# Performance work log

Hardware: AMD Instinct MI355X
Metric: run time of the kernel (lower is better)

The kernel has to match this reference:

```python
import jax, jax.numpy as jnp
import numpy as np
from jax import lax

D = 256      # key/query dim
D_F = 256    # diff feature channels
C_TOK = 1    # leading context tokens in query_vit
EPS = 1e-6


def conv2d(x, w, b, pad):
    out = lax.conv_general_dilated(x, w, (1, 1), [(pad, pad), (pad, pad)],
                                   dimension_numbers=('NCHW', 'OIHW', 'NCHW'))
    return out + b[None, :, None, None]


def gn1(x, g, b):
    # GroupNorm with 1 group: normalize over (C,H,W) per sample
    mu = jnp.mean(x, axis=(1, 2, 3), keepdims=True)
    var = jnp.var(x, axis=(1, 2, 3), keepdims=True)
    xn = (x - mu) * lax.rsqrt(var + EPS)
    return xn * g[None, :, None, None] + b[None, :, None, None]


def resize_bilinear_ac(x, Ho, Wo):
    # F.interpolate(mode='bilinear', align_corners=True)
    B, C, H, W = x.shape
    ys = jnp.linspace(0.0, H - 1.0, Ho)
    xs = jnp.linspace(0.0, W - 1.0, Wo)
    y0 = jnp.floor(ys).astype(jnp.int32)
    y1 = jnp.minimum(y0 + 1, H - 1)
    wy = (ys - y0)[None, None, :, None]
    x0 = jnp.floor(xs).astype(jnp.int32)
    x1 = jnp.minimum(x0 + 1, W - 1)
    wx = (xs - x0)[None, None, None, :]
    r = x[:, :, y0, :] * (1.0 - wy) + x[:, :, y1, :] * wy
    return r[:, :, :, x0] * (1.0 - wx) + r[:, :, :, x1] * wx


def setup_inputs() -> dict:
    key = jax.random.key(0)
    ks = jax.random.split(key, 12)
    B, Hd, Wd, Ht, Wt = 8, 64, 64, 32, 32

    def kaiming(k, shape, fan_in):
        return jax.random.normal(k, shape, jnp.float32) * np.sqrt(2.0 / fan_in)

    return {
        'query_vit': jax.random.normal(ks[0], (B, C_TOK + Ht * Wt, D), jnp.float32),
        'feat_diff_cat': jax.random.normal(ks[1], (B, 5 * D_F, Hd, Wd), jnp.float32),
        'rb_w1': kaiming(ks[2], (D_F, 5 * D_F, 3, 3), 5 * D_F * 9), 'rb_b1': jnp.zeros((D_F,), jnp.float32),
        'rb_w2': kaiming(ks[3], (D_F, D_F, 3, 3), D_F * 9), 'rb_b2': jnp.zeros((D_F,), jnp.float32),
        'rb_ws': kaiming(ks[4], (D_F, 5 * D_F, 1, 1), 5 * D_F), 'rb_bs': jnp.zeros((D_F,), jnp.float32),
        'ln_g': jnp.ones((D_F,), jnp.float32), 'ln_b': jnp.zeros((D_F,), jnp.float32),
        'key_w': kaiming(ks[5], (D, D_F, 1, 1), D_F), 'key_b': jnp.zeros((D,), jnp.float32),
        'val_w': kaiming(ks[6], (D_F, D_F, 1, 1), D_F), 'val_b': jnp.zeros((D_F,), jnp.float32),
        'dh0_w': kaiming(ks[7], (D_F, D_F, 3, 3), D_F * 9), 'dh0_b': jnp.zeros((D_F,), jnp.float32),
        'dh1_w': kaiming(ks[8], (D_F, D_F, 3, 3), D_F * 9), 'dh1_b': jnp.zeros((D_F,), jnp.float32),
    }


def reference(query_vit, feat_diff_cat, rb_w1, rb_b1, rb_w2, rb_b2, rb_ws, rb_bs,
              ln_g, ln_b, key_w, key_b, val_w, val_b, dh0_w, dh0_b, dh1_w, dh1_b):
    B, _, h_diff, w_diff = feat_diff_cat.shape
    N = query_vit.shape[1] - C_TOK
    h_trm = w_trm = int(N ** 0.5)

    # ResBlock_ysh(D_f*5 -> D_f): conv3x3 + relu + conv3x3, 1x1-projected residual
    h = jax.nn.relu(conv2d(feat_diff_cat, rb_w1, rb_b1, 1))
    h = conv2d(h, rb_w2, rb_b2, 1)
    feat_diff = jax.nn.relu(h + conv2d(feat_diff_cat, rb_ws, rb_bs, 0))

    fln = gn1(feat_diff, ln_g, ln_b)
    key_diff = conv2d(fln, key_w, key_b, 0).reshape(B, D, -1)          # (B, D, HW)
    value_diff = conv2d(fln, val_w, val_b, 0).reshape(B, D_F, -1)      # (B, Df, HW)
    value_diff = jnp.transpose(value_diff, (0, 2, 1))                  # (B, HW, Df)

    # cross attention: (B, C+N, D) @ (B, D, HW) -> softmax -> @ (B, HW, Df)
    scores = jnp.einsum('bnd,bdm->bnm', query_vit, key_diff) * (D ** -0.5)
    attn = jax.nn.softmax(scores, axis=-1)
    out_cross = jnp.einsum('bnm,bmf->bnf', attn, value_diff)           # (B, C+N, Df)

    out_cross_c = out_cross[:, :C_TOK, :]
    out_p = jnp.transpose(out_cross[:, C_TOK:, :], (0, 2, 1)).reshape(B, D_F, h_trm, w_trm)
    out_p = jax.nn.relu(conv2d(out_p, dh0_w, dh0_b, 1))
    out_p = resize_bilinear_ac(out_p, h_diff, w_diff)
    out_p = out_p + feat_diff                                          # DropPath(0) = identity
    out_p = jax.nn.relu(conv2d(gn1(out_p, ln_g, ln_b), dh1_w, dh1_b, 1)) + out_p
    return out_cross_c, out_p
```

## Files before the change

kernel.cpp:

```cpp
#include <hip/hip_runtime.h>
#include <cstdint>
#include <cstddef>

typedef __attribute__((ext_vector_type(4))) float     f32x4;
typedef __attribute__((ext_vector_type(8))) __bf16    bf16x8;
typedef __attribute__((ext_vector_type(8))) short     short8;
typedef __attribute__((ext_vector_type(4))) unsigned short u16x4;
typedef unsigned short u16;

__device__ __forceinline__ float b2f(u16 u) {
  unsigned x = ((unsigned)u) << 16;
  float f;
  __builtin_memcpy(&f, &x, 4);
  return f;
}
__device__ __forceinline__ u16 f2b(float f) {
  unsigned u;
  __builtin_memcpy(&u, &f, 4);
  return (u16)((u + 0x7FFFu + ((u >> 16) & 1u)) >> 16);
}

struct GP {
  const u16*  A;
  const u16*  B;
  const float* bias;
  const void* aux;
  void*       C;
  float*      out0;
  long long   aBS, bBS, cBS, auxBS;
  int Ktot, Mrows, ldc;
  int cin, logW, wpad, poff;
  float scale;
};

#define GLDS16(g, l)                                                        \
  __builtin_amdgcn_global_load_lds(                                         \
      (const void __attribute__((address_space(1)))*)(g),                   \
      (void __attribute__((address_space(3)))*)(l), 16, 0, 0)

template <int AMODE, int CW, bool RELU>
__global__ __launch_bounds__(512, 2) void k_gemm8(GP gp) {
  const int tid = threadIdx.x;
  const int l = tid & 63, w = tid >> 6;
  const int b = blockIdx.z;
  const int m0 = blockIdx.x * 128;
  const int wm = w >> 2, wn = w & 3;

  __shared__ __align__(16) u16 sm[3][24576];

  f32x4 acc[4][4];
#pragma unroll
  for (int i = 0; i < 4; ++i)
#pragma unroll
    for (int j = 0; j < 4; ++j) acc[i][j] = (f32x4){0.f, 0.f, 0.f, 0.f};

  const u16* Ab = gp.A + (size_t)b * gp.aBS;
  const u16* Bb = gp.B + (size_t)b * gp.bBS;
  const int scoff = (((tid & 7) ^ ((tid >> 3) & 7)) << 3);

  const u16* aP[2];
  const u16* bP[4];
#pragma unroll
  for (int i = 0; i < 2; ++i) {
    const int p = m0 + i * 64 + (tid >> 3);
    if (AMODE == 0) {
      const int pc = p < gp.Mrows ? p : gp.Mrows - 1;
      aP[i] = Ab + (size_t)pc * gp.Ktot + scoff;
    } else {
      const int y = p >> gp.logW, x = p & ((1 << gp.logW) - 1);
      aP[i] = Ab + (size_t)((y + gp.poff) * gp.wpad + (x + gp.poff)) * gp.cin +
              scoff;
    }
  }
#pragma unroll
  for (int i = 0; i < 4; ++i)
    bP[i] = Bb + (size_t)(i * 64 + (tid >> 3)) * gp.Ktot + scoff;

  const int NT = gp.Ktot >> 6;
  int kcS = 0, tapS = 0, dxS = 0, ktS = 0;

  auto adv = [&](int& kA, int& kB) {
    kB = ktS << 6;
    if (AMODE == 0) {
      kA = ktS << 6;
    } else {
      kA = tapS * gp.cin + kcS;
      kcS += 64;
      if (kcS == gp.cin) {
        kcS = 0; ++dxS; ++tapS;
        if (dxS == 3) { dxS = 0; tapS += gp.wpad - 3; }
      }
    }
    ++ktS;
  };

#pragma unroll
  for (int pt = 0; pt < 2; ++pt) {
    int kA, kB;
    adv(kA, kB);
    u16* sA = &sm[pt][0] + (w << 9);
    u16* sB = &sm[pt][8192] + (w << 9);
    GLDS16(aP[0] + kA, sA);
    GLDS16(aP[1] + kA, sA + 4096);
    GLDS16(bP[0] + kB, sB);
    GLDS16(bP[1] + kB, sB + 4096);
    GLDS16(bP[2] + kB, sB + 8192);
    GLDS16(bP[3] + kB, sB + 12288);
  }
  asm volatile("s_waitcnt vmcnt(6)" ::: "memory");
  __builtin_amdgcn_s_barrier();

  const int lr = l & 15, lc = l >> 4;
  int bufC = 0, bufS = 2;

  for (int t = 0; t < NT; ++t) {
    const u16* sAc = &sm[bufC][0];
    const u16* sBc = &sm[bufC][8192];
    const bool sOK = (t + 2 < NT);
    int kAs = 0, kBs = 0;
    if (sOK) adv(kAs, kBs);
    u16* sAs = &sm[bufS][0] + (w << 9);
    u16* sBs = &sm[bufS][8192] + (w << 9);

    bf16x8 bv[4][2];
    {
      bf16x8 av[2][2];
#pragma unroll
      for (int mi = 0; mi < 2; ++mi) {
        const int row = wm * 64 + mi * 16 + lr;
#pragma unroll
        for (int ks = 0; ks < 2; ++ks) {
          const int cc = ks * 4 + lc;
          av[mi][ks] =
              *(const bf16x8*)(sAc + row * 64 + ((cc ^ (row & 7)) << 3));
        }
      }
#pragma unroll
      for (int ni = 0; ni < 4; ++ni) {
        const int row = wn * 64 + ni * 16 + lr;
#pragma unroll
        for (int ks = 0; ks < 2; ++ks) {
          const int cc = ks * 4 + lc;
          bv[ni][ks] =
              *(const bf16x8*)(sBc + row * 64 + ((cc ^ (row & 7)) << 3));
        }
      }
      if (sOK) {
        GLDS16(aP[0] + kAs, sAs);
        GLDS16(aP[1] + kAs, sAs + 4096);
        GLDS16(bP[0] + kBs, sBs);
      }
      __builtin_amdgcn_s_barrier();
      asm volatile("s_waitcnt lgkmcnt(0)" ::: "memory");
      __builtin_amdgcn_sched_barrier(0);
      __builtin_amdgcn_s_setprio(1);
#pragma unroll
      for (int ks = 0; ks < 2; ++ks)
#pragma unroll
        for (int mi = 0; mi < 2; ++mi)
#pragma unroll
          for (int ni = 0; ni < 4; ++ni)
            acc[mi][ni] = __builtin_amdgcn_mfma_f32_16x16x32_bf16(
                av[mi][ks], bv[ni][ks], acc[mi][ni], 0, 0, 0);
      __builtin_amdgcn_sched_barrier(0);
      __builtin_amdgcn_s_setprio(0);
    }
    __builtin_amdgcn_s_barrier();
    {
      bf16x8 av[2][2];
#pragma unroll
      for (int mi = 0; mi < 2; ++mi) {
        const int row = wm * 64 + (mi + 2) * 16 + lr;
#pragma unroll
        for (int ks = 0; ks < 2; ++ks) {
          const int cc = ks * 4 + lc;
          av[mi][ks] =
              *(const bf16x8*)(sAc + row * 64 + ((cc ^ (row & 7)) << 3));
        }
      }
      if (sOK) {
        GLDS16(bP[1] + kBs, sBs + 4096);
        GLDS16(bP[2] + kBs, sBs + 8192);
        GLDS16(bP[3] + kBs, sBs + 12288);
      }
      __builtin_amdgcn_s_barrier();
      asm volatile("s_waitcnt lgkmcnt(0)" ::: "memory");
      __builtin_amdgcn_sched_barrier(0);
      __builtin_amdgcn_s_setprio(1);
#pragma unroll
      for (int ks = 0; ks < 2; ++ks)
#pragma unroll
        for (int mi = 0; mi < 2; ++mi)
#pragma unroll
          for (int ni = 0; ni < 4; ++ni)
            acc[mi + 2][ni] = __builtin_amdgcn_mfma_f32_16x16x32_bf16(
                av[mi][ks], bv[ni][ks], acc[mi + 2][ni], 0, 0, 0);
      __builtin_amdgcn_sched_barrier(0);
      __builtin_amdgcn_s_setprio(0);
    }
    if (t + 1 < NT) {
      if (t + 2 < NT)
        asm volatile("s_waitcnt vmcnt(6)" ::: "memory");
      else
        asm volatile("s_waitcnt vmcnt(0)" ::: "memory");
      __builtin_amdgcn_s_barrier();
    }
    bufC = bufC == 2 ? 0 : bufC + 1;
    bufS = bufS == 2 ? 0 : bufS + 1;
  }

#pragma unroll
  for (int mi = 0; mi < 4; ++mi) {
#pragma unroll
    for (int ni = 0; ni < 4; ++ni) {
      const int ncol = wn * 64 + ni * 16 + lr;
      const int mbase = m0 + wm * 64 + mi * 16 + lc * 4;
      const float bv_ = gp.bias ? gp.bias[ncol] : 0.f;
      if constexpr (CW == 0) {
#pragma unroll
        for (int r = 0; r < 4; ++r) {
          float v = acc[mi][ni][r] + bv_;
          if (RELU) v = fmaxf(v, 0.f);
          ((u16*)gp.C)[(size_t)b * gp.cBS + (size_t)(mbase + r) * 256 + ncol] =
              f2b(v);
        }
      } else if constexpr (CW == 1) {
#pragma unroll
        for (int r = 0; r < 4; ++r) {
          float v = acc[mi][ni][r] + bv_;
          if (RELU) v = fmaxf(v, 0.f);
          const int mrow = mbase + r;
          const int y = mrow >> 6, x = mrow & 63;
          ((u16*)gp.C)[(size_t)b * gp.cBS +
                       (size_t)((y + 1) * 66 + x + 1) * 256 + ncol] = f2b(v);
        }
      } else if constexpr (CW == 2) {
#pragma unroll
        for (int r = 0; r < 4; ++r) {
          const int mrow = mbase + r;
          const float s =
              b2f(((const u16*)gp.aux)[(size_t)b * gp.auxBS +
                                       (size_t)mrow * 256 + ncol]);
          float v = acc[mi][ni][r] + bv_ + s;
          v = fmaxf(v, 0.f);
          ((float*)gp.C)[(size_t)b * gp.cBS + (size_t)mrow * 256 + ncol] = v;
        }
      } else if constexpr (CW == 6) {
        float* Cf =
            (float*)gp.C + (size_t)b * gp.cBS + (size_t)ncol * 4096 + mbase;
        const float* mid = (const float*)gp.aux + (size_t)b * gp.auxBS;
        f32x4 o;
#pragma unroll
        for (int r = 0; r < 4; ++r) {
          float v = acc[mi][ni][r] + bv_;
          v = fmaxf(v, 0.f);
          o[r] = v + mid[(size_t)(mbase + r) * 256 + ncol];
        }
        *(f32x4*)Cf = o;
      }
    }
  }
}

template <int AMODE, int CW, bool RELU>
__global__ __launch_bounds__(256, 2) void k_gemm(GP gp) {
  const int tid = threadIdx.x;
  const int l = tid & 63, w = tid >> 6;
  const int b = blockIdx.z;
  const int m0 = blockIdx.x * 128, n0 = blockIdx.y * 128;
  const int wm = w >> 1, wn = w & 1;

  __shared__ __align__(16) u16 smA[128 * 64];
  __shared__ __align__(16) u16 smB[128 * 64];

  f32x4 acc[4][4];
#pragma unroll
  for (int i = 0; i < 4; ++i)
#pragma unroll
    for (int j = 0; j < 4; ++j) acc[i][j] = (f32x4){0.f, 0.f, 0.f, 0.f};

  const u16* Ab = gp.A + (size_t)b * gp.aBS;
  const u16* Bb = gp.B + (size_t)b * gp.bBS;

  const int scoff = (((l & 7) ^ (l >> 3)) << 3);

  const u16* aRow[4];
  const u16* bRow[4];
  u16* ldsA[4];
  u16* ldsB[4];
#pragma unroll
  for (int i = 0; i < 4; ++i) {
    const int r = w * 32 + i * 8 + (l >> 3);
    bRow[i] = Bb + (size_t)(n0 + r) * gp.Ktot + scoff;
    const int p = m0 + r;
    if (AMODE == 0) {
      const int pc = p < gp.Mrows ? p : gp.Mrows - 1;
      aRow[i] = Ab + (size_t)pc * gp.Ktot + scoff;
    } else {
      const int y = p >> gp.logW, x = p & ((1 << gp.logW) - 1);
      const int icoord = (y + gp.poff) * gp.wpad + (x + gp.poff);
      aRow[i] = Ab + (size_t)icoord * gp.cin + scoff;
    }
    ldsA[i] = smA + (w * 32 + i * 8) * 64;
    ldsB[i] = smB + (w * 32 + i * 8) * 64;
  }

  const int ktiles = gp.Ktot >> 6;
  int tap_off = 0, dx = 0, kc = 0;

  for (int kt = 0; kt < ktiles; ++kt) {
    int koffA;
    if (AMODE == 0)
      koffA = kt << 6;
    else
      koffA = tap_off * gp.cin + kc;
    const int koffB = kt << 6;
#pragma unroll
    for (int i = 0; i < 4; ++i) GLDS16(aRow[i] + koffA, ldsA[i]);
#pragma unroll
    for (int i = 0; i < 4; ++i) GLDS16(bRow[i] + koffB, ldsB[i]);

    if (AMODE == 1) {
      kc += 64;
      if (kc == gp.cin) {
        kc = 0;
        ++dx;
        ++tap_off;
        if (dx == 3) { dx = 0; tap_off += gp.wpad - 3; }
      }
    }

    __syncthreads();
#pragma unroll
    for (int ks = 0; ks < 2; ++ks) {
      bf16x8 av[4], bv[4];
      const int cc = (ks << 2) + (l >> 4);
#pragma unroll
      for (int mi = 0; mi < 4; ++mi) {
        const int row = wm * 64 + mi * 16 + (l & 15);
        av[mi] = *(const bf16x8*)((const char*)smA + (row << 7) +
                                  ((cc ^ (row & 7)) << 4));
      }
#pragma unroll
      for (int ni = 0; ni < 4; ++ni) {
        const int row = wn * 64 + ni * 16 + (l & 15);
        bv[ni] = *(const bf16x8*)((const char*)smB + (row << 7) +
                                  ((cc ^ (row & 7)) << 4));
      }
#pragma unroll
      for (int mi = 0; mi < 4; ++mi)
#pragma unroll
        for (int ni = 0; ni < 4; ++ni)
          acc[mi][ni] = __builtin_amdgcn_mfma_f32_16x16x32_bf16(
              av[mi], bv[ni], acc[mi][ni], 0, 0, 0);
    }
    __syncthreads();
  }

#pragma unroll
  for (int mi = 0; mi < 4; ++mi) {
#pragma unroll
    for (int ni = 0; ni < 4; ++ni) {
      const int ncol = n0 + wn * 64 + ni * 16 + (l & 15);
      const int mbase = m0 + wm * 64 + mi * 16 + ((l >> 4) << 2);
      const float bv_ = gp.bias ? gp.bias[ncol] : 0.f;

      if constexpr (CW == 3) {
        u16* Cu = (u16*)gp.C + (size_t)b * gp.cBS + (size_t)ncol * 4096 + mbase;
        u16x4 pk;
#pragma unroll
        for (int r = 0; r < 4; ++r) pk[r] = f2b(acc[mi][ni][r] + bv_);
        *(u16x4*)Cu = pk;
      } else if constexpr (CW == 7) {
        u16* base = (u16*)gp.C;
        if (ncol < 256) {
#pragma unroll
          for (int r = 0; r < 4; ++r)
            base[(size_t)b * 1048576 + (size_t)(mbase + r) * 256 + ncol] =
                f2b(acc[mi][ni][r] + bv_);
        } else {
          u16x4 pk;
#pragma unroll
          for (int r = 0; r < 4; ++r) pk[r] = f2b(acc[mi][ni][r] + bv_);
          *(u16x4*)(base + 8388608 + (size_t)b * 1048576 +
                    (size_t)(ncol - 256) * 4096 + mbase) = pk;
        }
      } else if constexpr (CW == 6) {
        float* Cf = (float*)gp.C + (size_t)b * gp.cBS + (size_t)ncol * 4096 + mbase;
        const float* mid = (const float*)gp.aux + (size_t)b * gp.auxBS;
        f32x4 o;
#pragma unroll
        for (int r = 0; r < 4; ++r) {
          float v = acc[mi][ni][r] + bv_;
          v = v > 0.f ? v : 0.f;
          o[r] = v + mid[(size_t)(mbase + r) * 256 + ncol];
        }
        *(f32x4*)Cf = o;
      } else {
#pragma unroll
        for (int reg = 0; reg < 4; ++reg) {
          const int mrow = mbase + reg;
          if (mrow >= gp.Mrows) continue;
          float v = acc[mi][ni][reg] * gp.scale + bv_;
          if (RELU) v = v > 0.f ? v : 0.f;
          if constexpr (CW == 0) {
            ((u16*)gp.C)[(size_t)b * gp.cBS + (size_t)mrow * gp.ldc + ncol] =
                f2b(v);
          } else if constexpr (CW == 2) {
            const float s =
                b2f(((const u16*)gp.aux)[(size_t)b * gp.auxBS +
                                         (size_t)mrow * 256 + ncol]);
            float v2 = v + s;
            v2 = v2 > 0.f ? v2 : 0.f;
            ((float*)gp.C)[(size_t)b * gp.cBS + (size_t)mrow * 256 + ncol] = v2;
          } else if constexpr (CW == 4) {
            if (mrow == 0) {
              gp.out0[(size_t)b * 256 + ncol] = v;
            } else {
              const int p = mrow - 1, y = p >> 5, x = p & 31;
              ((u16*)gp.C)[(size_t)b * gp.cBS +
                           (size_t)((y + 1) * 34 + (x + 1)) * 256 + ncol] =
                  f2b(v);
            }
          } else if constexpr (CW == 5) {
            ((float*)gp.C)[(size_t)b * gp.cBS + (size_t)mrow * 256 + ncol] = v;
          }
        }
      }
    }
  }
}


__global__ __launch_bounds__(256) void k_prep_x(const float* __restrict__ x,
                                                u16* __restrict__ o) {
  __shared__ float t[32][65];
  const int b = blockIdx.z, c0 = blockIdx.y << 5, y = blockIdx.x;
  const float* src = x + ((size_t)b * 1280 + c0) * 4096 + (size_t)y * 64;
#pragma unroll
  for (int i = 0; i < 8; ++i) {
    const int idx = threadIdx.x + (i << 8);
    const int c = idx >> 6, xx = idx & 63;
    t[c][xx] = src[(size_t)c * 4096 + xx];
  }
  __syncthreads();
  u16* dst = o + ((size_t)b * 4356 + (size_t)(y + 1) * 66 + 1) * 1280 + c0;
#pragma unroll
  for (int i = 0; i < 8; ++i) {
    const int idx = threadIdx.x + (i << 8);
    const int xx = idx >> 5, c = idx & 31;
    dst[(size_t)xx * 1280 + c] = f2b(t[c][xx]);
  }
}

__global__ __launch_bounds__(256) void k_zero_border(u16* __restrict__ p,
                                                     int P, int C) {
  const int per_img = (4 * P - 4) * C;
  const int total = 8 * per_img;
  for (int idx = blockIdx.x * 256 + threadIdx.x; idx < total;
       idx += gridDim.x * 256) {
    const int b = idx / per_img;
    const int r = idx % per_img;
    const int pix = r / C, c = r % C;
    int y, x;
    const int Pm = P - 1;
    if (pix < P) { y = 0; x = pix; }
    else if (pix < 2 * P) { y = Pm; x = pix - P; }
    else if (pix < 3 * P - 2) { y = pix - 2 * P + 1; x = 0; }
    else { y = pix - (3 * P - 2) + 1; x = Pm; }
    p[((size_t)b * P * P + (size_t)y * P + x) * C + c] = 0;
  }
}

__global__ __launch_bounds__(256) void k_prep_w3(const float* __restrict__ w,
                                                 u16* __restrict__ o, int cin,
                                                 int n) {
  for (int i = blockIdx.x * 256 + threadIdx.x; i < n; i += gridDim.x * 256) {
    const int ci = i % cin;
    const int r = i / cin;
    const int t = r % 9;
    const int co = r / 9;
    o[i] = f2b(w[((size_t)co * cin + ci) * 9 + t]);
  }
}

__global__ __launch_bounds__(256) void k_f2b(const float* __restrict__ x,
                                             u16* __restrict__ o, int n) {
  for (int i = blockIdx.x * 256 + threadIdx.x; i < n; i += gridDim.x * 256)
    o[i] = f2b(x[i]);
}

__global__ __launch_bounds__(256) void k_gn_stats(const float* __restrict__ x,
                                                  float* __restrict__ st) {
  const int b = blockIdx.y;
  const f32x4* xb = (const f32x4*)(x + (size_t)b * 1048576);
  float s = 0.f, s2 = 0.f;
  for (int i = blockIdx.x * 256 + threadIdx.x; i < 262144;
       i += gridDim.x * 256) {
    const f32x4 v = xb[i];
    s += v[0] + v[1] + v[2] + v[3];
    s2 += v[0] * v[0] + v[1] * v[1] + v[2] * v[2] + v[3] * v[3];
  }
#pragma unroll
  for (int o = 32; o; o >>= 1) {
    s += __shfl_down(s, o);
    s2 += __shfl_down(s2, o);
  }
  __shared__ float ls[4], ls2[4];
  const int w = threadIdx.x >> 6;
  if ((threadIdx.x & 63) == 0) { ls[w] = s; ls2[w] = s2; }
  __syncthreads();
  if (threadIdx.x == 0) {
    atomicAdd(&st[b * 2], ls[0] + ls[1] + ls[2] + ls[3]);
    atomicAdd(&st[b * 2 + 1], ls2[0] + ls2[1] + ls2[2] + ls2[3]);
  }
}

template <bool PAD>
__global__ __launch_bounds__(256) void k_gn_norm(const float* __restrict__ x,
                                                 const float* __restrict__ st,
                                                 const float* __restrict__ g,
                                                 const float* __restrict__ bb,
                                                 u16* __restrict__ o) {
  const int b = blockIdx.y;
  const float mu = st[b * 2] * (1.f / 1048576.f);
  const float var = st[b * 2 + 1] * (1.f / 1048576.f) - mu * mu;
  const float rs = rsqrtf(var + 1e-6f);
  const int i4 = blockIdx.x * 256 + threadIdx.x;
  const f32x4 v = ((const f32x4*)(x + (size_t)b * 1048576))[i4];
  const int flat = i4 << 2;
  const int c = flat & 255;
  const int p = flat >> 8;
  const f32x4 gv = *(const f32x4*)(g + c);
  const f32x4 bv = *(const f32x4*)(bb + c);
  u16x4 r;
#pragma unroll
  for (int k = 0; k < 4; ++k) r[k] = f2b((v[k] - mu) * rs * gv[k] + bv[k]);
  size_t oidx;
  if (PAD) {
    const int y = p >> 6, xx = p & 63;
    oidx = ((size_t)b * 4356 + (size_t)(y + 1) * 66 + xx + 1) * 256 + c;
  } else {
    oidx = ((size_t)b * 4096 + p) * 256 + c;
  }
  *(u16x4*)(o + oidx) = r;
}

__global__ __launch_bounds__(256) void k_softmax(u16* __restrict__ s) {
  const size_t row = blockIdx.x;
  u16* p = s + row * 4096;
  const int t = threadIdx.x;
  const short8 r0 = ((const short8*)p)[t];
  const short8 r1 = ((const short8*)p)[t + 256];
  float v[16];
#pragma unroll
  for (int i = 0; i < 8; ++i) {
    v[i] = b2f((u16)r0[i]);
    v[8 + i] = b2f((u16)r1[i]);
  }
  float m = v[0];
#pragma unroll
  for (int i = 1; i < 16; ++i) m = fmaxf(m, v[i]);
#pragma unroll
  for (int o = 32; o; o >>= 1) m = fmaxf(m, __shfl_xor(m, o));
  __shared__ float lm[4], lsum[4];
  const int w = t >> 6;
  if ((t & 63) == 0) lm[w] = m;
  __syncthreads();
  m = fmaxf(fmaxf(lm[0], lm[1]), fmaxf(lm[2], lm[3]));
  float sum = 0.f;
#pragma unroll
  for (int i = 0; i < 16; ++i) {
    v[i] = __expf(v[i] - m);
    sum += v[i];
  }
#pragma unroll
  for (int o = 32; o; o >>= 1) sum += __shfl_xor(sum, o);
  if ((t & 63) == 0) lsum[w] = sum;
  __syncthreads();
  sum = lsum[0] + lsum[1] + lsum[2] + lsum[3];
  const float inv = 1.f / sum;
  short8 o0, o1;
#pragma unroll
  for (int i = 0; i < 8; ++i) {
    o0[i] = (short)f2b(v[i] * inv);
    o1[i] = (short)f2b(v[8 + i] * inv);
  }
  ((short8*)p)[t] = o0;
  ((short8*)p)[t + 256] = o1;
}

__global__ __launch_bounds__(256) void k_resize_add(const float* __restrict__ d0,
                                                    const float* __restrict__ F,
                                                    float* __restrict__ mid) {
  const int i4 = blockIdx.x * 256 + threadIdx.x;
  const int flat = i4 << 2;
  const int c = flat & 255;
  const int p = (flat >> 8) & 4095;
  const int b = flat >> 20;
  const int y = p >> 6, x = p & 63;
  const float fy = y * (31.f / 63.f);
  const int y0 = (int)fy;
  const float wy = fy - y0;
  const int y1 = y0 + 1 > 31 ? 31 : y0 + 1;
  const float fx = x * (31.f / 63.f);
  const int x0 = (int)fx;
  const float wx = fx - x0;
  const int x1 = x0 + 1 > 31 ? 31 : x0 + 1;
  const float* db = d0 + (size_t)b * 262144;
  const f32x4 a = *(const f32x4*)(db + ((size_t)(y0 * 32 + x0) << 8) + c);
  const f32x4 bq = *(const f32x4*)(db + ((size_t)(y0 * 32 + x1) << 8) + c);
  const f32x4 cq = *(const f32x4*)(db + ((size_t)(y1 * 32 + x0) << 8) + c);
  const f32x4 dq = *(const f32x4*)(db + ((size_t)(y1 * 32 + x1) << 8) + c);
  f32x4 r = (a * (1.f - wx) + bq * wx) * (1.f - wy) +
            (cq * (1.f - wx) + dq * wx) * wy;
  r += *(const f32x4*)(F + (size_t)flat);
  *(f32x4*)(mid + (size_t)flat) = r;
}


extern "C" void kernel_launch(void* const* d_in, const int* in_sizes, int n_in,
                              void* d_out, int out_size, void* d_ws,
                              size_t ws_size, hipStream_t stream) {
  (void)in_sizes; (void)n_in; (void)out_size;

  const float* q   = (const float*)d_in[0];
  const float* xdc = (const float*)d_in[1];
  const float* w1  = (const float*)d_in[2];
  const float* b1  = (const float*)d_in[3];
  const float* w2  = (const float*)d_in[4];
  const float* b2  = (const float*)d_in[5];
  const float* wsc = (const float*)d_in[6];
  const float* bsc = (const float*)d_in[7];
  const float* lng = (const float*)d_in[8];
  const float* lnb = (const float*)d_in[9];
  const float* wk  = (const float*)d_in[10];
  const float* bk  = (const float*)d_in[11];
  const float* wv  = (const float*)d_in[12];
  const float* bv  = (const float*)d_in[13];
  const float* wd0 = (const float*)d_in[14];
  const float* bd0 = (const float*)d_in[15];
  const float* wd1 = (const float*)d_in[16];
  const float* bd1 = (const float*)d_in[17];

  char* ws = (char*)d_ws;
  size_t cur = 0;
  auto alloc = [&](size_t sz) {
    char* p = ws + cur;
    cur += sz;
    return p;
  };
  u16* XPAD = (u16*)alloc(89194496);
  u16* W1R  = (u16*)alloc(5898240);
  u16* W2R  = (u16*)alloc(1179648);
  u16* WSR  = (u16*)alloc(655360);
  u16* WKV  = (u16*)alloc(262144);
  float* BKV = (float*)alloc(2048);
  u16* WD0R = (u16*)alloc(1179648);
  u16* WD1R = (u16*)alloc(1179648);
  u16* SB   = (u16*)alloc(16777216);
  u16* H1   = (u16*)alloc(17842176);
  float* F  = (float*)alloc(33554432);
  u16* FLN  = (u16*)alloc(16777216);
  u16* KT   = (u16*)alloc(16777216);
  u16* V    = (u16*)alloc(16777216);
  u16* QB   = (u16*)alloc(4198400);
  u16* OCP  = (u16*)alloc(4734976);
  float* D0O = (float*)alloc(8388608);
  float* MID = (float*)alloc(33554432);
  u16* G2   = (u16*)alloc(17842176);
  float* ST = (float*)alloc(256);
  u16* SCORES = XPAD;
  (void)V;

  if (ws_size < cur) return;

  float* out0 = (float*)d_out;
  float* out1 = (float*)d_out + 2048;

  hipMemsetAsync(ST, 0, 256, stream);
  hipMemcpyAsync(BKV, bk, 1024, hipMemcpyDeviceToDevice, stream);
  hipMemcpyAsync(BKV + 256, bv, 1024, hipMemcpyDeviceToDevice, stream);

  k_zero_border<<<2048, 256, 0, stream>>>(XPAD, 66, 1280);
  k_zero_border<<<1024, 256, 0, stream>>>(H1, 66, 256);
  k_zero_border<<<1024, 256, 0, stream>>>(G2, 66, 256);
  k_zero_border<<<512, 256, 0, stream>>>(OCP, 34, 256);

  k_prep_x<<<dim3(64, 40, 8), 256, 0, stream>>>(xdc, XPAD);
  k_prep_w3<<<2048, 256, 0, stream>>>(w1, W1R, 1280, 2949120);
  k_prep_w3<<<1024, 256, 0, stream>>>(w2, W2R, 256, 589824);
  k_prep_w3<<<1024, 256, 0, stream>>>(wd0, WD0R, 256, 589824);
  k_prep_w3<<<1024, 256, 0, stream>>>(wd1, WD1R, 256, 589824);
  k_f2b<<<512, 256, 0, stream>>>(wsc, WSR, 327680);
  k_f2b<<<128, 256, 0, stream>>>(wk, WKV, 65536);
  k_f2b<<<128, 256, 0, stream>>>(wv, WKV + 65536, 65536);
  k_f2b<<<2048, 256, 0, stream>>>(q, QB, 2099200);

  const dim3 g8(32, 1, 8);
  {
    GP g{};
    g.A = XPAD; g.B = WSR; g.bias = bsc; g.C = SB;
    g.aBS = 5575680; g.bBS = 0; g.cBS = 1048576;
    g.Ktot = 1280; g.Mrows = 4096; g.ldc = 256;
    g.cin = 1280; g.logW = 6; g.wpad = 66; g.poff = 1; g.scale = 1.f;
    k_gemm8<1, 0, false><<<g8, 512, 0, stream>>>(g);
  }
  {
    GP g{};
    g.A = XPAD; g.B = W1R; g.bias = b1; g.C = H1;
    g.aBS = 5575680; g.bBS = 0; g.cBS = 1115136;
    g.Ktot = 11520; g.Mrows = 4096; g.ldc = 256;
    g.cin = 1280; g.logW = 6; g.wpad = 66; g.poff = 0; g.scale = 1.f;
    k_gemm8<1, 1, true><<<g8, 512, 0, stream>>>(g);
  }
  {
    GP g{};
    g.A = H1; g.B = W2R; g.bias = b2; g.C = F; g.aux = SB;
    g.aBS = 1115136; g.bBS = 0; g.cBS = 1048576; g.auxBS = 1048576;
    g.Ktot = 2304; g.Mrows = 4096; g.ldc = 256;
    g.cin = 256; g.logW = 6; g.wpad = 66; g.poff = 0; g.scale = 1.f;
    k_gemm8<1, 2, false><<<g8, 512, 0, stream>>>(g);
  }
  k_gn_stats<<<dim3(64, 8), 256, 0, stream>>>(F, ST);
  k_gn_norm<false><<<dim3(1024, 8), 256, 0, stream>>>(F, ST, lng, lnb, FLN);
  {
    GP g{};
    g.A = FLN; g.B = WKV; g.bias = BKV; g.C = KT;
    g.aBS = 1048576; g.bBS = 0; g.cBS = 0;
    g.Ktot = 256; g.Mrows = 4096; g.ldc = 256; g.scale = 1.f;
    k_gemm<0, 7, false><<<dim3(32, 4, 8), 256, 0, stream>>>(g);
  }
  {
    GP g{};
    g.A = QB; g.B = KT; g.bias = nullptr; g.C = SCORES;
    g.aBS = 262400; g.bBS = 1048576; g.cBS = 4198400;
    g.Ktot = 256; g.Mrows = 1025; g.ldc = 4096; g.scale = 0.0625f;
    k_gemm<0, 0, false><<<dim3(9, 32, 8), 256, 0, stream>>>(g);
  }
  k_softmax<<<8200, 256, 0, stream>>>(SCORES);
  {
    GP g{};
    g.A = SCORES; g.B = V; g.bias = nullptr; g.C = OCP; g.out0 = out0;
    g.aBS = 4198400; g.bBS = 1048576; g.cBS = 295936;
    g.Ktot = 4096; g.Mrows = 1025; g.ldc = 256; g.scale = 1.f;
    k_gemm<0, 4, false><<<dim3(9, 2, 8), 256, 0, stream>>>(g);
  }
  {
    GP g{};
    g.A = OCP; g.B = WD0R; g.bias = bd0; g.C = D0O;
    g.aBS = 295936; g.bBS = 0; g.cBS = 262144;
    g.Ktot = 2304; g.Mrows = 1024; g.ldc = 256;
    g.cin = 256; g.logW = 5; g.wpad = 34; g.poff = 0; g.scale = 1.f;
    k_gemm<1, 5, true><<<dim3(8, 2, 8), 256, 0, stream>>>(g);
  }
  k_resize_add<<<8192, 256, 0, stream>>>(D0O, F, MID);
  k_gn_stats<<<dim3(64, 8), 256, 0, stream>>>(MID, ST + 16);
  k_gn_norm<true><<<dim3(1024, 8), 256, 0, stream>>>(MID, ST + 16, lng, lnb, G2);
  {
    GP g{};
    g.A = G2; g.B = WD1R; g.bias = bd1; g.C = out1; g.aux = MID;
    g.aBS = 1115136; g.bBS = 0; g.cBS = 1048576; g.auxBS = 1048576;
    g.Ktot = 2304; g.Mrows = 4096; g.ldc = 256;
    g.cin = 256; g.logW = 6; g.wpad = 66; g.poff = 0; g.scale = 1.f;
    k_gemm8<1, 6, false><<<g8, 512, 0, stream>>>(g);
  }
}
```

Before: 743.7 us.

## Use 256x256-tile split-K GEMM for the big 3x3 conv with separate reduction

Replaces the 128-row GEMM for the 1280-channel 3x3 conv with a new kernel using 256x256 output tiles, double-buffered LDS and a two-way split-K, writing fp32 partials into the reused FLN buffer. A separate reduction kernel sums the two partials, adds bias, applies ReLU and writes padded bf16 H1. The larger tile improves operand reuse, and split-K keeps the grid at 256 blocks. The cost is extra fp32 partial traffic plus a reduce launch. It also moves the query conversion and OCP border zeroing after the conv and removes the now-unused epilogue variants.

```diff
diff --git a/kernel.cpp b/kernel.cpp
--- a/kernel.cpp
+++ b/kernel.cpp
@@ -37,6 +37,243 @@
   __builtin_amdgcn_global_load_lds(                                         \
       (const void __attribute__((address_space(1)))*)(g),                   \
       (void __attribute__((address_space(3)))*)(l), 16, 0, 0)
+
+struct G256 {
+  const u16* A;
+  const u16* B;
+  float* P;
+  long long aBS;
+  int Ktot, cin, logW, wpad, poff;
+};
+
+__global__ __launch_bounds__(512, 2) void k_gemm256(G256 gp) {
+  const int tid = threadIdx.x;
+  const int l = tid & 63, w = tid >> 6;
+  const int lr = l & 15, lc = l >> 4;
+  const int mt = blockIdx.x, sp = blockIdx.y, b = blockIdx.z;
+  const int m0 = mt << 8;
+  const int wm = w >> 2, wn = w & 3;
+
+  __shared__ __align__(16) u16 sm[2][32768];
+  u16* smb = &sm[0][0];
+
+  f32x4 acc[8][4];
+#pragma unroll
+  for (int i = 0; i < 8; ++i)
+#pragma unroll
+    for (int j = 0; j < 4; ++j) acc[i][j] = (f32x4){0.f, 0.f, 0.f, 0.f};
+
+  const u16* Ab = gp.A + (size_t)b * gp.aBS;
+  const int slot = l & 3;
+  const u16* aS[2];
+  const u16* bS[2];
+#pragma unroll
+  for (int j = 0; j < 2; ++j) {
+    const int r = j * 128 + w * 16 + (l >> 2);
+    const int p = m0 + r;
+    const int y = p >> gp.logW, x = p & ((1 << gp.logW) - 1);
+    const int sw = (slot ^ ((r >> 1) & 3)) << 3;
+    aS[j] = Ab + (size_t)((y + gp.poff) * gp.wpad + (x + gp.poff)) * gp.cin + sw;
+    bS[j] = gp.B + (size_t)r * gp.Ktot + sw;
+  }
+  auto dstA = [&](int buf, int ks, int j) -> u16* {
+    return smb + buf * 32768 + ks * 8192 + (j * 128 + w * 16) * 32 + l * 8;
+  };
+  auto dstB = [&](int buf, int ks, int j) -> u16* {
+    return smb + buf * 32768 + 16384 + ks * 8192 + (j * 128 + w * 16) * 32 + l * 8;
+  };
+
+  const int Thalf = (gp.Ktot >> 6) >> 1;
+  const int kt0 = sp * Thalf;
+  int off = kt0 << 6;
+  int tap = off / gp.cin;
+  int kcS = off - tap * gp.cin;
+  int dxS = tap % 3;
+  int tapS = (tap / 3) * gp.wpad + dxS;
+  int ktS = kt0;
+
+  auto adv = [&](int& kA, int& kB) {
+    kB = ktS << 6;
+    kA = tapS * gp.cin + kcS;
+    kcS += 64;
+    if (kcS == gp.cin) {
+      kcS = 0; ++dxS; ++tapS;
+      if (dxS == 3) { dxS = 0; tapS += gp.wpad - 3; }
+    }
+    ++ktS;
+  };
+
+  {
+    int kA, kB;
+    adv(kA, kB);
+    GLDS16(aS[0] + kA, dstA(0, 0, 0));
+    GLDS16(aS[1] + kA, dstA(0, 0, 1));
+    GLDS16(bS[0] + kB, dstB(0, 0, 0));
+    GLDS16(bS[1] + kB, dstB(0, 0, 1));
+    GLDS16(aS[0] + kA + 32, dstA(0, 1, 0));
+    GLDS16(aS[1] + kA + 32, dstA(0, 1, 1));
+    GLDS16(bS[0] + kB + 32, dstB(0, 1, 0));
+    GLDS16(bS[1] + kB + 32, dstB(0, 1, 1));
+  }
+  asm volatile("s_waitcnt vmcnt(4)" ::: "memory");
+  __builtin_amdgcn_s_barrier();
+
+  const int NT = Thalf;
+  for (int t = 0; t < NT; ++t) {
+    const int buf = t & 1;
+    const char* base = (const char*)smb + buf * 65536;
+    const bool pf = (t + 1 < NT);
+    int kA = 0, kB = 0;
+    if (pf) adv(kA, kB);
+
+    bf16x8 av[4], bv[4];
+
+#pragma unroll
+    for (int mi = 0; mi < 4; ++mi) {
+      const int row = wm * 128 + mi * 16 + lr;
+      av[mi] = *(const bf16x8*)(base + row * 64 + ((lc ^ ((row >> 1) & 3)) << 4));
+    }
+#pragma unroll
+    for (int ni = 0; ni < 4; ++ni) {
+      const int row = wn * 64 + ni * 16 + lr;
+      bv[ni] = *(const bf16x8*)(base + 32768 + row * 64 +
+                                ((lc ^ ((row >> 1) & 3)) << 4));
+    }
+    if (pf) {
+      GLDS16(aS[0] + kA, dstA(buf ^ 1, 0, 0));
+      GLDS16(aS[1] + kA, dstA(buf ^ 1, 0, 1));
+    }
+    __builtin_amdgcn_s_barrier();
+    asm volatile("s_waitcnt lgkmcnt(0)" ::: "memory");
+    __builtin_amdgcn_sched_barrier(0);
+    __builtin_amdgcn_s_setprio(1);
+#pragma unroll
+    for (int mi = 0; mi < 4; ++mi)
+#pragma unroll
+      for (int ni = 0; ni < 4; ++ni)
+        acc[mi][ni] = __builtin_amdgcn_mfma_f32_16x16x32_bf16(
+            av[mi], bv[ni], acc[mi][ni], 0, 0, 0);
+    __builtin_amdgcn_s_setprio(0);
+    __builtin_amdgcn_sched_barrier(0);
+    __builtin_amdgcn_s_barrier();
+
+#pragma unroll
+    for (int mi = 0; mi < 4; ++mi) {
+      const int row = wm * 128 + (4 + mi) * 16 + lr;
+      av[mi] = *(const bf16x8*)(base + row * 64 + ((lc ^ ((row >> 1) & 3)) << 4));
+    }
+    if (pf) {
+      GLDS16(bS[0] + kB, dstB(buf ^ 1, 0, 0));
+      GLDS16(bS[1] + kB, dstB(buf ^ 1, 0, 1));
+    }
+    __builtin_amdgcn_s_barrier();
+    asm volatile("s_waitcnt lgkmcnt(0)" ::: "memory");
+    __builtin_amdgcn_sched_barrier(0);
+    __builtin_amdgcn_s_setprio(1);
+#pragma unroll
+    for (int mi = 0; mi < 4; ++mi)
+#pragma unroll
+      for (int ni = 0; ni < 4; ++ni)
+        acc[4 + mi][ni] = __builtin_amdgcn_mfma_f32_16x16x32_bf16(
+            av[mi], bv[ni], acc[4 + mi][ni], 0, 0, 0);
+    __builtin_amdgcn_s_setprio(0);
+    __builtin_amdgcn_sched_barrier(0);
+    if (pf)
+      asm volatile("s_waitcnt vmcnt(4)" ::: "memory");
+    else
+      asm volatile("s_waitcnt vmcnt(0)" ::: "memory");
+    __builtin_amdgcn_s_barrier();
+
+#pragma unroll
+    for (int mi = 0; mi < 4; ++mi) {
+      const int row = wm * 128 + mi * 16 + lr;
+      av[mi] = *(const bf16x8*)(base + 16384 + row * 64 +
+                                ((lc ^ ((row >> 1) & 3)) << 4));
+    }
+#pragma unroll
+    for (int ni = 0; ni < 4; ++ni) {
+      const int row = wn * 64 + ni * 16 + lr;
+      bv[ni] = *(const bf16x8*)(base + 49152 + row * 64 +
+                                ((lc ^ ((row >> 1) & 3)) << 4));
+    }
+    if (pf) {
+      GLDS16(aS[0] + kA + 32, dstA(buf ^ 1, 1, 0));
+      GLDS16(aS[1] + kA + 32, dstA(buf ^ 1, 1, 1));
+    }
+    __builtin_amdgcn_s_barrier();
+    asm volatile("s_waitcnt lgkmcnt(0)" ::: "memory");
+    __builtin_amdgcn_sched_barrier(0);
+    __builtin_amdgcn_s_setprio(1);
+#pragma unroll
+    for (int mi = 0; mi < 4; ++mi)
+#pragma unroll
+      for (int ni = 0; ni < 4; ++ni)
+        acc[mi][ni] = __builtin_amdgcn_mfma_f32_16x16x32_bf16(
+            av[mi], bv[ni], acc[mi][ni], 0, 0, 0);
+    __builtin_amdgcn_s_setprio(0);
+    __builtin_amdgcn_sched_barrier(0);
+    __builtin_amdgcn_s_barrier();
+
+#pragma unroll
+    for (int mi = 0; mi < 4; ++mi) {
+      const int row = wm * 128 + (4 + mi) * 16 + lr;
+      av[mi] = *(const bf16x8*)(base + 16384 + row * 64 +
+                                ((lc ^ ((row >> 1) & 3)) << 4));
+    }
+    if (pf) {
+      GLDS16(bS[0] + kB + 32, dstB(buf ^ 1, 1, 0));
+      GLDS16(bS[1] + kB + 32, dstB(buf ^ 1, 1, 1));
+    }
+    __builtin_amdgcn_s_barrier();
+    asm volatile("s_waitcnt lgkmcnt(0)" ::: "memory");
+    __builtin_amdgcn_sched_barrier(0);
+    __builtin_amdgcn_s_setprio(1);
+#pragma unroll
+    for (int mi = 0; mi < 4; ++mi)
+#pragma unroll
+      for (int ni = 0; ni < 4; ++ni)
+        acc[4 + mi][ni] = __builtin_amdgcn_mfma_f32_16x16x32_bf16(
+            av[mi], bv[ni], acc[4 + mi][ni], 0, 0, 0);
+    __builtin_amdgcn_s_setprio(0);
+    __builtin_amdgcn_sched_barrier(0);
+    if (pf) {
+      asm volatile("s_waitcnt vmcnt(4)" ::: "memory");
+      __builtin_amdgcn_s_barrier();
+    }
+  }
+
+  float* P = gp.P + ((size_t)sp * 128 + b * 16 + mt) * 65536;
+#pragma unroll
+  for (int mi = 0; mi < 8; ++mi)
+#pragma unroll
+    for (int ni = 0; ni < 4; ++ni) {
+      const int ncol = wn * 64 + ni * 16 + lr;
+      const int mloc = wm * 128 + mi * 16 + lc * 4;
+#pragma unroll
+      for (int r = 0; r < 4; ++r)
+        P[(size_t)(mloc + r) * 256 + ncol] = acc[mi][ni][r];
+    }
+}
+
+__global__ __launch_bounds__(256) void k_reduceH1(const float* __restrict__ P,
+                                                  const float* __restrict__ bias,
+                                                  u16* __restrict__ o) {
+  const int i4 = blockIdx.x * 256 + threadIdx.x;
+  const int flat = i4 << 2;
+  const int n0 = flat & 255;
+  const int mloc = (flat >> 8) & 255;
+  const int gm = flat >> 16;
+  const f32x4 a = *(const f32x4*)(P + (size_t)gm * 65536 + mloc * 256 + n0);
+  const f32x4 c = *(const f32x4*)(P + (size_t)(128 + gm) * 65536 + mloc * 256 + n0);
+  const f32x4 bb = *(const f32x4*)(bias + n0);
+  const int batch = gm >> 4;
+  const int mg = (gm & 15) * 256 + mloc;
+  const int y = mg >> 6, x = mg & 63;
+  u16x4 r;
+#pragma unroll
+  for (int k = 0; k < 4; ++k) r[k] = f2b(fmaxf(a[k] + c[k] + bb[k], 0.f));
+  *(u16x4*)(o + ((size_t)batch * 4356 + (size_t)(y + 1) * 66 + x + 1) * 256 + n0) = r;
+}
 
 template <int AMODE, int CW, bool RELU>
 __global__ __launch_bounds__(512, 2) void k_gemm8(GP gp) {
@@ -385,17 +622,6 @@
           *(u16x4*)(base + 8388608 + (size_t)b * 1048576 +
                     (size_t)(ncol - 256) * 4096 + mbase) = pk;
         }
-      } else if constexpr (CW == 6) {
-        float* Cf = (float*)gp.C + (size_t)b * gp.cBS + (size_t)ncol * 4096 + mbase;
-        const float* mid = (const float*)gp.aux + (size_t)b * gp.auxBS;
-        f32x4 o;
-#pragma unroll
-        for (int r = 0; r < 4; ++r) {
-          float v = acc[mi][ni][r] + bv_;
-          v = v > 0.f ? v : 0.f;
-          o[r] = v + mid[(size_t)(mbase + r) * 256 + ncol];
-        }
-        *(f32x4*)Cf = o;
       } else {
 #pragma unroll
         for (int reg = 0; reg < 4; ++reg) {
@@ -406,13 +632,6 @@
           if constexpr (CW == 0) {
             ((u16*)gp.C)[(size_t)b * gp.cBS + (size_t)mrow * gp.ldc + ncol] =
                 f2b(v);
-          } else if constexpr (CW == 2) {
-            const float s =
-                b2f(((const u16*)gp.aux)[(size_t)b * gp.auxBS +
-                                         (size_t)mrow * 256 + ncol]);
-            float v2 = v + s;
-            v2 = v2 > 0.f ? v2 : 0.f;
-            ((float*)gp.C)[(size_t)b * gp.cBS + (size_t)mrow * 256 + ncol] = v2;
           } else if constexpr (CW == 4) {
             if (mrow == 0) {
               gp.out0[(size_t)b * 256 + ncol] = v;
@@ -671,6 +890,7 @@
   u16* G2   = (u16*)alloc(17842176);
   float* ST = (float*)alloc(256);
   u16* SCORES = XPAD;
+  float* PART = (float*)FLN;
   (void)V;
 
   if (ws_size < cur) return;
@@ -685,7 +905,6 @@
   k_zero_border<<<2048, 256, 0, stream>>>(XPAD, 66, 1280);
   k_zero_border<<<1024, 256, 0, stream>>>(H1, 66, 256);
   k_zero_border<<<1024, 256, 0, stream>>>(G2, 66, 256);
-  k_zero_border<<<512, 256, 0, stream>>>(OCP, 34, 256);
 
   k_prep_x<<<dim3(64, 40, 8), 256, 0, stream>>>(xdc, XPAD);
   k_prep_w3<<<2048, 256, 0, stream>>>(w1, W1R, 1280, 2949120);
@@ -695,7 +914,6 @@
   k_f2b<<<512, 256, 0, stream>>>(wsc, WSR, 327680);
   k_f2b<<<128, 256, 0, stream>>>(wk, WKV, 65536);
   k_f2b<<<128, 256, 0, stream>>>(wv, WKV + 65536, 65536);
-  k_f2b<<<2048, 256, 0, stream>>>(q, QB, 2099200);
 
   const dim3 g8(32, 1, 8);
   {
@@ -707,13 +925,16 @@
     k_gemm8<1, 0, false><<<g8, 512, 0, stream>>>(g);
   }
   {
-    GP g{};
-    g.A = XPAD; g.B = W1R; g.bias = b1; g.C = H1;
-    g.aBS = 5575680; g.bBS = 0; g.cBS = 1115136;
-    g.Ktot = 11520; g.Mrows = 4096; g.ldc = 256;
-    g.cin = 1280; g.logW = 6; g.wpad = 66; g.poff = 0; g.scale = 1.f;
-    k_gemm8<1, 1, true><<<g8, 512, 0, stream>>>(g);
-  }
+    G256 g{};
+    g.A = XPAD; g.B = W1R; g.P = PART;
+    g.aBS = 5575680; g.Ktot = 11520;
+    g.cin = 1280; g.logW = 6; g.wpad = 66; g.poff = 0;
+    k_gemm256<<<dim3(16, 2, 8), 512, 0, stream>>>(g);
+    k_reduceH1<<<8192, 256, 0, stream>>>(PART, b1, H1);
+  }
+  k_f2b<<<2048, 256, 0, stream>>>(q, QB, 2099200);
+  k_zero_border<<<512, 256, 0, stream>>>(OCP, 34, 256);
+
   {
     GP g{};
     g.A = H1; g.B = W2R; g.bias = b2; g.C = F; g.aux = SB;
```

New measurement: 724.2 us. 2.6% less time.
